# Kernel tuning notes

Measured on AMD Instinct MI355X. Metric: run time of the kernel, lower is better.

Reference implementation:

```python
import jax, jax.numpy as jnp
import numpy as np
from jax import lax

ALPHA = float(np.exp(-1.0 / 5.0))   # exp(-1/tau_mem), tau_mem=5.0
THRESHOLD = 1.0


def _dwconv(x, w, b, groups):
    # x: (B, Cin, T), w: (Cout, Cin/groups, K), 'same' padding for odd K
    pad = (w.shape[-1] - 1) // 2
    y = lax.conv_general_dilated(
        x, w, window_strides=(1,), padding=[(pad, pad)],
        dimension_numbers=("NCH", "OIH", "NCH"), feature_group_count=groups)
    return y + b[None, :, None]


def setup_inputs() -> dict:
    key = jax.random.key(0)
    ks = jax.random.split(key, 12)
    B, C, T = 8, 256, 4096
    OP = 6            # out_per_kernel for each of the 3 kernel sizes
    DEC = 128         # decoder_channels
    f32 = jnp.float32
    d = {}
    d["x"] = jax.random.normal(ks[0], (B, C, T), f32)
    # depthwise multi-path conv params (groups=C): weight (C*OP, 1, K)
    d["w3"] = jax.random.normal(ks[1], (C * OP, 1, 3), f32) * 0.2
    d["b3"] = jnp.zeros((C * OP,), f32)
    d["w5"] = jax.random.normal(ks[2], (C * OP, 1, 5), f32) * 0.15
    d["b5"] = jnp.zeros((C * OP,), f32)
    d["w9"] = jax.random.normal(ks[3], (C * OP, 1, 9), f32) * 0.1
    d["b9"] = jnp.zeros((C * OP,), f32)
    # reduce: Conv1d(C*18 -> C, k=1, groups=C): weight (C, 18, 1)
    d["w_red"] = jax.random.normal(ks[4], (C, 3 * OP, 1), f32) * 0.2
    d["b_red"] = jnp.zeros((C,), f32)
    d["latency_scale"] = jnp.asarray(5.0, f32)
    # output_gates: xavier uniform (C, C) with zero diagonal
    bound = float(np.sqrt(6.0 / (C + C)))
    og = jax.random.uniform(ks[5], (C, C), f32, -bound, bound)
    d["output_gates"] = og * (1.0 - jnp.eye(C, dtype=f32))
    d["bias"] = jnp.zeros((C,), f32)
    # post_mlp: Linear(C, DEC) -> ReLU -> Linear(DEC, C); stored as (in, out)
    d["W1"] = jax.random.normal(ks[6], (C, DEC), f32) * float(np.sqrt(2.0 / C))
    d["b1"] = jnp.zeros((DEC,), f32)
    d["W2"] = jax.random.normal(ks[7], (DEC, C), f32) * float(np.sqrt(2.0 / DEC))
    d["b2"] = jnp.zeros((C,), f32)
    return d


def reference(x, w3, b3, w5, b5, w9, b9, w_red, b_red,
              latency_scale, output_gates, bias, W1, b1, W2, b2):
    B, C, T = x.shape
    # DepthwiseMultiPathEncoder: 3 depthwise convs -> cat -> grouped 1x1 reduce
    o3 = _dwconv(x, w3, b3, C)
    o5 = _dwconv(x, w5, b5, C)
    o9 = _dwconv(x, w9, b9, C)
    cat = jnp.concatenate([o3, o5, o9], axis=1)      # (B, 18C, T)
    drive = _dwconv(cat, w_red, b_red, C)             # (B, C, T)
    # LIF membrane recurrence + first-spike latency (sequential over T)
    d_t = jnp.moveaxis(drive, 2, 0)                   # (T, B, C)
    def step(V, dt):
        V = ALPHA * V + (1.0 - ALPHA) * dt
        return V, V >= THRESHOLD
    _, crossed = lax.scan(step, jnp.zeros((B, C), x.dtype), d_t)  # (T, B, C) bool
    fired_any = crossed.any(axis=0)
    first_t = jnp.argmax(crossed, axis=0)             # first True index
    true_latency = jnp.where(fired_any, first_t, T).astype(x.dtype)  # (B, C)
    # latency -> activation -> gated mix -> MLP -> softplus, clamp [0, T]
    scale = jnp.maximum(latency_scale, 0.001)
    act = jnp.exp(-true_latency / scale)              # (B, C)
    mixed = act @ output_gates.T + bias[None, :]      # (B, C)
    h = jax.nn.relu(mixed @ W1 + b1)
    raw_pred = h @ W2 + b2
    pred_latency = jnp.clip(jax.nn.softplus(raw_pred), 0.0, float(T))
    return pred_latency, true_latency, act
```

## Files before the change

kernel.cpp:

```cpp
#include <hip/hip_runtime.h>
#include <math.h>

#define C_CH 256
#define T_LEN 4096


template <int K>
__device__ inline void fold_bundle(const float* __restrict__ wp,
                                   const float* __restrict__ bp,
                                   const float* __restrict__ wred6,
                                   int p0, float* __restrict__ w9, float& bacc)
{
    const int off = (9 - K) >> 1;
    #pragma unroll
    for (int k = 0; k < 9; ++k) w9[k] = 0.0f;
    #pragma unroll
    for (int j = 0; j < 6; ++j) {
        const float wr = wred6[j];
        bacc += wr * bp[p0 + j];
        #pragma unroll
        for (int k = 0; k < K; ++k)
            w9[off + k] += wr * wp[(p0 + j) * K + k];
    }
}

__global__ __launch_bounds__(256) void fold_kernel(
    const float* __restrict__ w3, const float* __restrict__ b3,
    const float* __restrict__ w5, const float* __restrict__ b5,
    const float* __restrict__ w9, const float* __restrict__ b9,
    const float* __restrict__ w_red, const float* __restrict__ b_red,
    float* __restrict__ ws)
{
    const int c = threadIdx.x;
    float wf[3][9];
    float bacc = 0.0f;
    #pragma unroll
    for (int r = 0; r < 3; ++r) {
        const int q0 = 18 * c + 6 * r;
        const float* wred6 = w_red + c * 18 + 6 * r;
        if (q0 < 1536)      fold_bundle<3>(w3, b3, wred6, q0,        wf[r], bacc);
        else if (q0 < 3072) fold_bundle<5>(w5, b5, wred6, q0 - 1536, wf[r], bacc);
        else                fold_bundle<9>(w9, b9, wred6, q0 - 3072, wf[r], bacc);
    }
    float* o = ws + c * 32;
    #pragma unroll
    for (int r = 0; r < 3; ++r)
        #pragma unroll
        for (int k = 0; k < 9; ++k) o[r * 9 + k] = wf[r][k];
    o[27] = b_red[c] + bacc;
    o[28] = 0.0f; o[29] = 0.0f; o[30] = 0.0f; o[31] = 0.0f;
}

__global__ __launch_bounds__(256) void drive_scan_kernel(
    const float* __restrict__ x, const float* __restrict__ ws,
    const float* __restrict__ latency_scale,
    float* __restrict__ out_lat, float* __restrict__ out_act)
{
    const int blk  = blockIdx.x;
    const int b    = blk >> 8;
    const int c    = blk & 255;
    const int tid  = threadIdx.x;
    const int lane = tid & 63;
    const int wv   = tid >> 6;

    __shared__ float sWaveTot[4];
    __shared__ float sCarry[4];
    __shared__ int   sMin[4];

    const int base = 16 * tid - 4;
    float xa[3][24];
    #pragma unroll
    for (int r = 0; r < 3; ++r) {
        const int q      = 18 * c + 6 * r;
        const int region = (q >= 1536) + (q >= 3072);
        const int srcc   = 3 * c + r - (region << 8);
        const float* xr  = x + ((size_t)b * C_CH + srcc) * T_LEN;
        if (tid > 0 && tid < 255) {
            const float4* p = (const float4*)(xr + base);
            #pragma unroll
            for (int v = 0; v < 6; ++v) {
                float4 q4 = p[v];
                xa[r][4 * v + 0] = q4.x; xa[r][4 * v + 1] = q4.y;
                xa[r][4 * v + 2] = q4.z; xa[r][4 * v + 3] = q4.w;
            }
        } else {
            #pragma unroll
            for (int e = 0; e < 24; ++e) {
                const int t = base + e;
                xa[r][e] = (t >= 0 && t < T_LEN) ? xr[t] : 0.0f;
            }
        }
    }

    const float* wc = ws + c * 32;
    const float Beff = wc[27];
    float d[16];
    #pragma unroll
    for (int tt = 0; tt < 16; ++tt) d[tt] = Beff;
    #pragma unroll
    for (int r = 0; r < 3; ++r) {
        #pragma unroll
        for (int k = 0; k < 9; ++k) {
            const float wk = wc[r * 9 + k];
            #pragma unroll
            for (int tt = 0; tt < 16; ++tt)
                d[tt] = fmaf(wk, xa[r][tt + k], d[tt]);
        }
    }

    const float A   = (float)0.8187307530779818;
    const float OMA = (float)(1.0 - 0.8187307530779818);

    float S = 0.0f;
    #pragma unroll
    for (int tt = 0; tt < 16; ++tt) S = A * S + OMA * d[tt];

    const float Fp[6] = {
        (float)4.0762203978366215e-02,
        (float)1.6615572731739337e-03,
        (float)2.7607725720371943e-06,
        (float)7.6218649302532563e-12,
        (float)5.8092835977683129e-23,
        (float)3.3744728758705166e-45
    };
    float cinc = S;
    #pragma unroll
    for (int s = 0; s < 6; ++s) {
        const int o = 1 << s;
        const float y = __shfl_up(cinc, o, 64);
        if (lane >= o) cinc = fmaf(Fp[s], y, cinc);
    }
    if (lane == 63) sWaveTot[wv] = cinc;
    __syncthreads();
    if (tid == 0) {
        float g = 0.0f;
        #pragma unroll
        for (int w = 0; w < 4; ++w) { sCarry[w] = g; g = sWaveTot[w]; }
    }
    __syncthreads();
    const float cprev = __shfl_up(cinc, 1, 64);
    const float Vin = (lane ? cprev : 0.0f)
                    + expf(-3.2f * (float)lane) * sCarry[wv];

    float V = Vin;
    int firstT = T_LEN;
    #pragma unroll
    for (int tt = 0; tt < 16; ++tt) {
        V = A * V + OMA * d[tt];
        if (V >= 1.0f && firstT == T_LEN) firstT = 16 * tid + tt;
    }

    #pragma unroll
    for (int o = 32; o > 0; o >>= 1)
        firstT = min(firstT, __shfl_xor(firstT, o, 64));
    if (lane == 0) sMin[wv] = firstT;
    __syncthreads();
    if (tid == 0) {
        const int f = min(min(sMin[0], sMin[1]), min(sMin[2], sMin[3]));
        const float lat   = (float)f;
        const float scale = fmaxf(latency_scale[0], 0.001f);
        out_lat[blk] = lat;
        out_act[blk] = expf(-lat / scale);
    }
}

__global__ __launch_bounds__(256) void mlp_kernel(
    const float* __restrict__ act,
    const float* __restrict__ og, const float* __restrict__ bias,
    const float* __restrict__ W1, const float* __restrict__ b1,
    const float* __restrict__ W2, const float* __restrict__ b2,
    float* __restrict__ out_pred)
{
    const int b = blockIdx.x;
    const int j = threadIdx.x;
    __shared__ float sAct[256];
    __shared__ float sMix[256];
    __shared__ float sH[128];

    sAct[j] = act[b * 256 + j];
    __syncthreads();

    float mix = bias[j];
    const float* ogr = og + (size_t)j * 256;
    #pragma unroll 8
    for (int i = 0; i < 256; ++i) mix = fmaf(sAct[i], ogr[i], mix);
    sMix[j] = mix;
    __syncthreads();

    if (j < 128) {
        float h = b1[j];
        #pragma unroll 8
        for (int i = 0; i < 256; ++i) h = fmaf(sMix[i], W1[i * 128 + j], h);
        sH[j] = fmaxf(h, 0.0f);
    }
    __syncthreads();

    float raw = b2[j];
    #pragma unroll 8
    for (int k = 0; k < 128; ++k) raw = fmaf(sH[k], W2[k * 256 + j], raw);

    const float sp = fmaxf(raw, 0.0f) + log1pf(expf(-fabsf(raw)));
    out_pred[b * 256 + j] = fminf(fmaxf(sp, 0.0f), 4096.0f);
}

extern "C" void kernel_launch(void* const* d_in, const int* in_sizes, int n_in,
                              void* d_out, int out_size, void* d_ws, size_t ws_size,
                              hipStream_t stream) {
    const float* x    = (const float*)d_in[0];
    const float* w3   = (const float*)d_in[1];
    const float* b3   = (const float*)d_in[2];
    const float* w5   = (const float*)d_in[3];
    const float* b5   = (const float*)d_in[4];
    const float* w9   = (const float*)d_in[5];
    const float* b9   = (const float*)d_in[6];
    const float* wred = (const float*)d_in[7];
    const float* bred = (const float*)d_in[8];
    const float* ls   = (const float*)d_in[9];
    const float* og   = (const float*)d_in[10];
    const float* bias = (const float*)d_in[11];
    const float* W1   = (const float*)d_in[12];
    const float* b1   = (const float*)d_in[13];
    const float* W2   = (const float*)d_in[14];
    const float* b2   = (const float*)d_in[15];

    float* ws       = (float*)d_ws;
    float* out      = (float*)d_out;
    float* out_pred = out;
    float* out_lat  = out + 2048;
    float* out_act  = out + 4096;

    fold_kernel<<<1, 256, 0, stream>>>(w3, b3, w5, b5, w9, b9, wred, bred, ws);
    drive_scan_kernel<<<2048, 256, 0, stream>>>(x, ws, ls, out_lat, out_act);
    mlp_kernel<<<8, 256, 0, stream>>>(out_act, og, bias, W1, b1, W2, b2, out_pred);
}
```

Before: 146.7 us.

## Fuse weight folding into scan kernel and share conv halos via LDS

Removes the separate single-block fold kernel: each block now folds its channel's 27 effective taps and bias into shared memory using 28 threads. The input loads change from overlapping 24-element float4 windows to 16-element aligned loads, with the 4-element halos exchanged between neighbouring threads through a shared-memory buffer. This saves one kernel launch and its serial dependency, and cuts redundant global reads. In exchange every block repeats the small fold computation and adds LDS traffic and a barrier.

```diff
diff --git a/kernel.cpp b/kernel.cpp
--- a/kernel.cpp
+++ b/kernel.cpp
@@ -5,54 +5,12 @@
 #define T_LEN 4096
 
 
-template <int K>
-__device__ inline void fold_bundle(const float* __restrict__ wp,
-                                   const float* __restrict__ bp,
-                                   const float* __restrict__ wred6,
-                                   int p0, float* __restrict__ w9, float& bacc)
-{
-    const int off = (9 - K) >> 1;
-    #pragma unroll
-    for (int k = 0; k < 9; ++k) w9[k] = 0.0f;
-    #pragma unroll
-    for (int j = 0; j < 6; ++j) {
-        const float wr = wred6[j];
-        bacc += wr * bp[p0 + j];
-        #pragma unroll
-        for (int k = 0; k < K; ++k)
-            w9[off + k] += wr * wp[(p0 + j) * K + k];
-    }
-}
-
-__global__ __launch_bounds__(256) void fold_kernel(
+__global__ __launch_bounds__(256) void drive_scan_kernel(
+    const float* __restrict__ x,
     const float* __restrict__ w3, const float* __restrict__ b3,
     const float* __restrict__ w5, const float* __restrict__ b5,
     const float* __restrict__ w9, const float* __restrict__ b9,
     const float* __restrict__ w_red, const float* __restrict__ b_red,
-    float* __restrict__ ws)
-{
-    const int c = threadIdx.x;
-    float wf[3][9];
-    float bacc = 0.0f;
-    #pragma unroll
-    for (int r = 0; r < 3; ++r) {
-        const int q0 = 18 * c + 6 * r;
-        const float* wred6 = w_red + c * 18 + 6 * r;
-        if (q0 < 1536)      fold_bundle<3>(w3, b3, wred6, q0,        wf[r], bacc);
-        else if (q0 < 3072) fold_bundle<5>(w5, b5, wred6, q0 - 1536, wf[r], bacc);
-        else                fold_bundle<9>(w9, b9, wred6, q0 - 3072, wf[r], bacc);
-    }
-    float* o = ws + c * 32;
-    #pragma unroll
-    for (int r = 0; r < 3; ++r)
-        #pragma unroll
-        for (int k = 0; k < 9; ++k) o[r * 9 + k] = wf[r][k];
-    o[27] = b_red[c] + bacc;
-    o[28] = 0.0f; o[29] = 0.0f; o[30] = 0.0f; o[31] = 0.0f;
-}
-
-__global__ __launch_bounds__(256) void drive_scan_kernel(
-    const float* __restrict__ x, const float* __restrict__ ws,
     const float* __restrict__ latency_scale,
     float* __restrict__ out_lat, float* __restrict__ out_act)
 {
@@ -63,48 +21,85 @@
     const int lane = tid & 63;
     const int wv   = tid >> 6;
 
+    __shared__ float sWF[28];
+    __shared__ float sHalo[3][8][256];
     __shared__ float sWaveTot[4];
     __shared__ float sCarry[4];
     __shared__ int   sMin[4];
 
-    const int base = 16 * tid - 4;
-    float xa[3][24];
+    const int t0 = tid << 4;
+    float xv[3][16];
     #pragma unroll
     for (int r = 0; r < 3; ++r) {
-        const int q      = 18 * c + 6 * r;
-        const int region = (q >= 1536) + (q >= 3072);
-        const int srcc   = 3 * c + r - (region << 8);
-        const float* xr  = x + ((size_t)b * C_CH + srcc) * T_LEN;
-        if (tid > 0 && tid < 255) {
-            const float4* p = (const float4*)(xr + base);
+        const int src = (3 * c + r) & 255;
+        const float4* p = (const float4*)(x + ((size_t)b * C_CH + src) * T_LEN + t0);
+        #pragma unroll
+        for (int v = 0; v < 4; ++v) {
+            float4 q = p[v];
+            xv[r][4 * v + 0] = q.x; xv[r][4 * v + 1] = q.y;
+            xv[r][4 * v + 2] = q.z; xv[r][4 * v + 3] = q.w;
+        }
+        #pragma unroll
+        for (int k = 0; k < 4; ++k) {
+            sHalo[r][k][tid]     = xv[r][k];
+            sHalo[r][4 + k][tid] = xv[r][12 + k];
+        }
+    }
+
+    if (tid < 27) {
+        const int r = tid / 9, k = tid - 9 * r;
+        const int q0     = 18 * c + 6 * r;
+        const int region = (q0 >= 1536) + (q0 >= 3072);
+        const int p0     = q0 - region * 1536;
+        const int K      = (region == 0) ? 3 : (region == 1 ? 5 : 9);
+        const int off    = (9 - K) >> 1;
+        const float* wP  = (region == 0) ? w3 : (region == 1 ? w5 : w9);
+        const int kk     = k - off;
+        float w = 0.0f;
+        if (kk >= 0 && kk < K) {
+            const float* wr = w_red + c * 18 + 6 * r;
             #pragma unroll
-            for (int v = 0; v < 6; ++v) {
-                float4 q4 = p[v];
-                xa[r][4 * v + 0] = q4.x; xa[r][4 * v + 1] = q4.y;
-                xa[r][4 * v + 2] = q4.z; xa[r][4 * v + 3] = q4.w;
-            }
-        } else {
+            for (int j = 0; j < 6; ++j)
+                w = fmaf(wr[j], wP[(p0 + j) * K + kk], w);
+        }
+        sWF[tid] = w;
+    } else if (tid == 27) {
+        float acc = b_red[c];
+        #pragma unroll
+        for (int r = 0; r < 3; ++r) {
+            const int q0     = 18 * c + 6 * r;
+            const int region = (q0 >= 1536) + (q0 >= 3072);
+            const int p0     = q0 - region * 1536;
+            const float* bP  = (region == 0) ? b3 : (region == 1 ? b5 : b9);
+            const float* wr  = w_red + c * 18 + 6 * r;
             #pragma unroll
-            for (int e = 0; e < 24; ++e) {
-                const int t = base + e;
-                xa[r][e] = (t >= 0 && t < T_LEN) ? xr[t] : 0.0f;
-            }
-        }
-    }
-
-    const float* wc = ws + c * 32;
-    const float Beff = wc[27];
+            for (int j = 0; j < 6; ++j) acc = fmaf(wr[j], bP[p0 + j], acc);
+        }
+        sWF[27] = acc;
+    }
+    __syncthreads();
+
+    const float Beff = sWF[27];
     float d[16];
     #pragma unroll
     for (int tt = 0; tt < 16; ++tt) d[tt] = Beff;
     #pragma unroll
     for (int r = 0; r < 3; ++r) {
+        float xa[24];
+        #pragma unroll
+        for (int e = 0; e < 4; ++e)
+            xa[e] = tid ? sHalo[r][4 + e][tid - 1] : 0.0f;
+        #pragma unroll
+        for (int e = 0; e < 16; ++e) xa[4 + e] = xv[r][e];
+        #pragma unroll
+        for (int e = 0; e < 4; ++e)
+            xa[20 + e] = (tid < 255) ? sHalo[r][e][tid + 1] : 0.0f;
         #pragma unroll
         for (int k = 0; k < 9; ++k) {
-            const float wk = wc[r * 9 + k];
+            const float wk = sWF[r * 9 + k];
             #pragma unroll
             for (int tt = 0; tt < 16; ++tt)
-                d[tt] = fmaf(wk, xa[r][tt + k], d[tt]);
+                d[tt] = fmaf(wk, xa[tt + k], d[tt]);
         }
     }
 
@@ -147,7 +142,7 @@
     #pragma unroll
     for (int tt = 0; tt < 16; ++tt) {
         V = A * V + OMA * d[tt];
-        if (V >= 1.0f && firstT == T_LEN) firstT = 16 * tid + tt;
+        if (V >= 1.0f && firstT == T_LEN) firstT = t0 + tt;
     }
 
     #pragma unroll
@@ -223,13 +218,12 @@
     const float* W2   = (const float*)d_in[14];
     const float* b2   = (const float*)d_in[15];
 
-    float* ws       = (float*)d_ws;
     float* out      = (float*)d_out;
     float* out_pred = out;
     float* out_lat  = out + 2048;
     float* out_act  = out + 4096;
 
-    fold_kernel<<<1, 256, 0, stream>>>(w3, b3, w5, b5, w9, b9, wred, bred, ws);
-    drive_scan_kernel<<<2048, 256, 0, stream>>>(x, ws, ls, out_lat, out_act);
+    drive_scan_kernel<<<2048, 256, 0, stream>>>(
+        x, w3, b3, w5, b5, w9, b9, wred, bred, ls, out_lat, out_act);
     mlp_kernel<<<8, 256, 0, stream>>>(out_act, og, bias, W1, b1, W2, b2, out_pred);
 }
```

After: 139.0 us. 5.2% less time.
